# Kernel tuning notes

Measured on AMD Instinct MI355X. Metric: run time of the kernel, lower is better.

The kernel has to match this reference:

```python
import jax, jax.numpy as jnp
import numpy as np

N = 50000      # nodes
E = 800000     # edges (before self-loops)
IN = 128       # in_channels
HID = 64       # hidden_channels
OUT = 64       # out_channels
G = 512        # number of graphs in the batch


def _glorot(key, shape):
    fan_in, fan_out = shape[0], shape[-1]
    s = jnp.sqrt(6.0 / (fan_in + fan_out))
    return jax.random.uniform(key, shape, jnp.float32, -s, s)


def setup_inputs() -> dict:
    key = jax.random.key(0)
    ks = jax.random.split(key, 16)
    x = jax.random.normal(ks[0], (N, IN), jnp.float32)
    edge_index = jax.random.randint(ks[1], (2, E), 0, N, jnp.int64)
    batch = jnp.sort(jax.random.randint(ks[2], (N,), 0, G, jnp.int64))
    return {
        "x": x,
        "edge_index": edge_index,
        "batch": batch,
        # GCNConv(IN, HID)
        "W1": _glorot(ks[3], (IN, HID)),
        "b1": jnp.zeros((HID,), jnp.float32),
        # GATConv(HID, HID, heads=2, concat=True)
        "W2": _glorot(ks[4], (HID, 2 * HID)),
        "a_src2": _glorot(ks[5], (2, HID)),
        "a_dst2": _glorot(ks[6], (2, HID)),
        "b2": jnp.zeros((2 * HID,), jnp.float32),
        # GATConv(2*HID, OUT, heads=1, concat=False)
        "W3": _glorot(ks[7], (2 * HID, OUT)),
        "a_src3": _glorot(ks[8], (1, OUT)),
        "a_dst3": _glorot(ks[9], (1, OUT)),
        "b3": jnp.zeros((OUT,), jnp.float32),
        # fc: Linear(OUT, 2)
        "Wfc": _glorot(ks[10], (OUT, 2)),
        "bfc": jnp.zeros((2,), jnp.float32),
    }


def _add_self_loops(src, dst, n):
    loop = jnp.arange(n, dtype=src.dtype)
    return jnp.concatenate([src, loop]), jnp.concatenate([dst, loop])


def _gcn_conv(x, src, dst, W, b):
    # src -> dst message passing with symmetric normalization (self-loops included)
    n = x.shape[0]
    h = x @ W                                      # [N, F]
    deg = jax.ops.segment_sum(jnp.ones(src.shape[0], h.dtype), dst, num_segments=n)
    dis = jnp.where(deg > 0, jax.lax.rsqrt(jnp.maximum(deg, 1e-12)), 0.0)
    norm = dis[src] * dis[dst]                     # [E']
    out = jax.ops.segment_sum(h[src] * norm[:, None], dst, num_segments=n)
    return out + b


def _gat_conv(x, src, dst, W, a_src, a_dst, b, heads, outc, concat):
    n = x.shape[0]
    h = (x @ W).reshape(n, heads, outc)            # [N, H, F]
    al_s = (h * a_src).sum(-1)                     # [N, H] from source nodes
    al_d = (h * a_dst).sum(-1)                     # [N, H] from target nodes
    e = jax.nn.leaky_relu(al_s[src] + al_d[dst], 0.2)   # [E', H]
    emax = jax.ops.segment_max(e, dst, num_segments=n)  # every node has a self-loop
    ex = jnp.exp(e - emax[dst])
    den = jax.ops.segment_sum(ex, dst, num_segments=n)
    alpha = ex / den[dst]                          # segment softmax over incoming edges
    out = jax.ops.segment_sum(h[src] * alpha[..., None], dst, num_segments=n)
    out = out.reshape(n, heads * outc) if concat else out.mean(axis=1)
    return out + b


def reference(x, edge_index, batch, W1, b1, W2, a_src2, a_dst2, b2,
              W3, a_src3, a_dst3, b3, Wfc, bfc):
    n = x.shape[0]
    src, dst = _add_self_loops(edge_index[0], edge_index[1], n)
    h = jax.nn.relu(_gcn_conv(x, src, dst, W1, b1))            # dropout = identity (eval)
    h = jax.nn.relu(_gat_conv(h, src, dst, W2, a_src2, a_dst2, b2, 2, HID, True))
    h = _gat_conv(h, src, dst, W3, a_src3, a_dst3, b3, 1, OUT, False)
    # global mean pool over graphs
    sums = jax.ops.segment_sum(h, batch, num_segments=G)
    cnts = jax.ops.segment_sum(jnp.ones((n,), h.dtype), batch, num_segments=G)
    pooled = sums / jnp.maximum(cnts, 1.0)[:, None]            # [G, OUT]
    logits = pooled @ Wfc + bfc                                # [G, 2]
    return jax.nn.log_softmax(logits, axis=1)
```

## Files before the change

kernel.cpp:

```cpp
#include <hip/hip_runtime.h>
#include <hip/hip_bf16.h>
#include <hip/hip_fp16.h>
#include <math.h>

#define BDIM 256

using v8h = __attribute__((ext_vector_type(8))) _Float16;
using v4f = __attribute__((ext_vector_type(4))) float;

#define NB  512
#define CH  8192
#define CAP 4096
#define PS  8


__device__ __forceinline__ float wave_max64(float v) {
#pragma unroll
  for (int o = 32; o > 0; o >>= 1) v = fmaxf(v, __shfl_xor(v, o, 64));
  return v;
}
__device__ __forceinline__ float wave_sum64(float v) {
#pragma unroll
  for (int o = 32; o > 0; o >>= 1) v += __shfl_xor(v, o, 64);
  return v;
}

__device__ __forceinline__ float leaky02(float v) {
  return v >= 0.0f ? v : 0.2f * v;
}

template <int KIN, int KOUT, bool A_FP32, int HEADS, bool SCALE>
__launch_bounds__(BDIM) __global__
void gemm_mfma(const void* __restrict__ Ap, const float* __restrict__ W,
               _Float16* __restrict__ C, const float* __restrict__ rs,
               const float* __restrict__ a_src, const float* __restrict__ a_dst,
               float* __restrict__ al_s, float* __restrict__ al_d, int N) {
  constexpr int KP = KIN + 8;
  constexpr int NT = KOUT / 16;
  __shared__ _Float16 Wt[KOUT * KP];
  int tid = threadIdx.x;
  for (int i = tid; i < KIN * KOUT; i += BDIM) {
    int k = i / KOUT, n = i % KOUT;
    Wt[n * KP + k] = (_Float16)W[i];
  }
  __syncthreads();
  int lane = tid & 63;
  int quad = lane >> 4, l16 = lane & 15;
  int m0 = blockIdx.x * 64 + (tid >> 6) * 16;
  if (m0 >= N) return;
  v4f acc[NT];
#pragma unroll
  for (int nt = 0; nt < NT; ++nt) acc[nt] = (v4f){0.0f, 0.0f, 0.0f, 0.0f};
#pragma unroll
  for (int k0 = 0; k0 < KIN; k0 += 32) {
    v8h a;
    if constexpr (A_FP32) {
      const float* ap = (const float*)Ap + (size_t)(m0 + l16) * KIN + k0 + quad * 8;
#pragma unroll
      for (int j = 0; j < 8; ++j) a[j] = (_Float16)ap[j];
    } else {
      a = *(const v8h*)((const _Float16*)Ap + (size_t)(m0 + l16) * KIN + k0 + quad * 8);
    }
#pragma unroll
    for (int nt = 0; nt < NT; ++nt) {
      v8h b = *(const v8h*)&Wt[(nt * 16 + l16) * KP + k0 + quad * 8];
      acc[nt] = __builtin_amdgcn_mfma_f32_16x16x32_f16(a, b, acc[nt], 0, 0, 0);
    }
  }
  float sc[4];
#pragma unroll
  for (int r = 0; r < 4; ++r) sc[r] = SCALE ? rs[m0 + quad * 4 + r] : 1.0f;
#pragma unroll
  for (int nt = 0; nt < NT; ++nt)
#pragma unroll
    for (int r = 0; r < 4; ++r)
      C[(size_t)(m0 + quad * 4 + r) * KOUT + nt * 16 + l16] =
          (_Float16)(acc[nt][r] * sc[r]);

  if constexpr (HEADS > 0) {
    constexpr int TPH = NT / HEADS;
    constexpr int FPH = KOUT / HEADS;
    float av_s[NT], av_d[NT];
#pragma unroll
    for (int nt = 0; nt < NT; ++nt) {
      int head = nt / TPH, c = (nt % TPH) * 16 + l16;
      av_s[nt] = a_src[head * FPH + c];
      av_d[nt] = a_dst[head * FPH + c];
    }
#pragma unroll
    for (int r = 0; r < 4; ++r) {
#pragma unroll
      for (int head = 0; head < HEADS; ++head) {
        float ps = 0.0f, pd = 0.0f;
#pragma unroll
        for (int t = 0; t < TPH; ++t) {
          int nt = head * TPH + t;
          ps += acc[nt][r] * av_s[nt];
          pd += acc[nt][r] * av_d[nt];
        }
#pragma unroll
        for (int o = 1; o < 16; o <<= 1) {
          ps += __shfl_xor(ps, o, 64);
          pd += __shfl_xor(pd, o, 64);
        }
        if (l16 == 0) {
          int row = m0 + quad * 4 + r;
          al_s[(size_t)head * N + row] = ps;
          al_d[(size_t)head * N + row] = pd;
        }
      }
    }
  }
}


__launch_bounds__(BDIM) __global__
void hist_a(const int* __restrict__ ei, int E, int TOT, int bw,
            int* __restrict__ counts, int nWG) {
  __shared__ int hist[NB];
  int tid = threadIdx.x, wg = blockIdx.x;
  for (int i = tid; i < NB; i += BDIM) hist[i] = 0;
  __syncthreads();
  int base = wg * CH, lim = min(CH, TOT - base);
  for (int i = tid; i < lim; i += BDIM) {
    int e = base + i;
    int dst = (e < E) ? ei[E + e] : (e - E);
    atomicAdd(&hist[dst / bw], 1);
  }
  __syncthreads();
  for (int b = tid; b < NB; b += BDIM) counts[(size_t)b * nWG + wg] = hist[b];
}

__launch_bounds__(BDIM) __global__
void scan_bucket(const int* __restrict__ counts, int nWG,
                 int* __restrict__ off, int* __restrict__ btot) {
  int b = blockIdx.x * (BDIM / 64) + (threadIdx.x >> 6);
  int lane = threadIdx.x & 63;
  if (b >= NB) return;
  const int* c = counts + (size_t)b * nWG;
  int* o = off + (size_t)b * nWG;
  int carry = 0;
  for (int base = 0; base < nWG; base += 64) {
    int i = base + lane;
    int v = (i < nWG) ? c[i] : 0;
    int incl = v;
#pragma unroll
    for (int s = 1; s < 64; s <<= 1) {
      int t = __shfl_up(incl, s, 64);
      if (lane >= s) incl += t;
    }
    if (i < nWG) o[i] = carry + incl - v;
    carry += __shfl(incl, 63, 64);
  }
  if (lane == 0) btot[b] = carry;
}

__launch_bounds__(512) __global__
void scan_tot(const int* __restrict__ btot, int* __restrict__ bbase,
              int* __restrict__ row_ptr, int N, int TOT) {
  __shared__ int wsum[8], wpre[8];
  int tid = threadIdx.x, lane = tid & 63, w = tid >> 6;
  int v = btot[tid];
  int incl = v;
#pragma unroll
  for (int o = 1; o < 64; o <<= 1) {
    int t = __shfl_up(incl, o, 64);
    if (lane >= o) incl += t;
  }
  if (lane == 63) wsum[w] = incl;
  __syncthreads();
  if (w == 0 && lane < 8) {
    int s = wsum[lane];
#pragma unroll
    for (int o = 1; o < 8; o <<= 1) {
      int t = __shfl_up(s, o, 64);
      if (lane >= o) s += t;
    }
    wpre[lane] = s - wsum[lane];
  }
  __syncthreads();
  bbase[tid] = wpre[w] + incl - v;
  if (tid == 0) { bbase[NB] = TOT; row_ptr[N] = TOT; }
}

__launch_bounds__(BDIM) __global__
void bucket_b(const int* __restrict__ ei, int E, int TOT, int bw,
              const int* __restrict__ off, const int* __restrict__ bbase,
              int nWG, unsigned int* __restrict__ ebuf) {
  __shared__ int cur[NB];
  int tid = threadIdx.x, wg = blockIdx.x;
  for (int b = tid; b < NB; b += BDIM)
    cur[b] = bbase[b] + off[(size_t)b * nWG + wg];
  __syncthreads();
  int base = wg * CH, lim = min(CH, TOT - base);
  for (int i = tid; i < lim; i += BDIM) {
    int e = base + i;
    int src, dst;
    if (e < E) { src = ei[e]; dst = ei[E + e]; }
    else       { src = dst = e - E; }
    int b = dst / bw;
    int pos = atomicAdd(&cur[b], 1);
    ebuf[pos] = ((unsigned int)(dst - b * bw) << 17) | (unsigned int)src;
  }
}

__launch_bounds__(BDIM) __global__
void csr_c(const unsigned int* __restrict__ ebuf, const int* __restrict__ bbase,
           int N, int bw,
           int* __restrict__ row_ptr, float* __restrict__ dis,
           int* __restrict__ csr_src) {
  __shared__ unsigned int eb[CAP];
  __shared__ unsigned int ob[CAP];
  __shared__ int cnt[128], loff[128], cur[128];
  int tid = threadIdx.x, b = blockIdx.x;
  int d0 = b * bw;
  if (d0 >= N) return;
  int width = min(bw, N - d0);
  int sbase = bbase[b];
  int send = bbase[b + 1];
  int nb = send - sbase;
  if (tid < 128) cnt[tid] = 0;
  __syncthreads();
  for (int i = tid; i < nb; i += BDIM) {
    unsigned int v = ebuf[sbase + i];
    eb[i] = v;
    atomicAdd(&cnt[v >> 17], 1);
  }
  __syncthreads();
  if (tid < 64) {
    int c0 = cnt[tid * 2], c1 = cnt[tid * 2 + 1];
    int s = c0 + c1;
    int incl = s;
#pragma unroll
    for (int o = 1; o < 64; o <<= 1) {
      int t = __shfl_up(incl, o, 64);
      if (tid >= o) incl += t;
    }
    int excl = incl - s;
    loff[tid * 2] = excl;
    loff[tid * 2 + 1] = excl + c0;
  }
  __syncthreads();
  if (tid < width) {
    row_ptr[d0 + tid] = sbase + loff[tid];
    dis[d0 + tid] = rsqrtf((float)cnt[tid]);
    cur[tid] = loff[tid];
  }
  __syncthreads();
  for (int i = tid; i < nb; i += BDIM) {
    unsigned int v = eb[i];
    int p = atomicAdd(&cur[v >> 17], 1);
    ob[p] = v & 0x1FFFFu;
  }
  __syncthreads();
  for (int i = tid; i < nb; i += BDIM) csr_src[sbase + i] = (int)ob[i];
}

__launch_bounds__(BDIM) __global__
void gcn_gather(const __half* __restrict__ h, const int* __restrict__ row_ptr,
                const int* __restrict__ csr_src, const float* __restrict__ dis,
                const float* __restrict__ b, __half* __restrict__ out, int N) {
  constexpr int U = 8;
  int wid = blockIdx.x * (BDIM / 64) + (threadIdx.x >> 6);
  int lane = threadIdx.x & 63;
  if (wid >= N) return;
  int beg = row_ptr[wid], end = row_ptr[wid + 1];
  float acc = 0.0f;
  for (int base = beg; base < end; base += 64) {
    int nch = min(64, end - base);
    int s_l = (lane < nch) ? csr_src[base + lane] : 0;
    int jfull = nch & ~(U - 1);
    for (int j = 0; j < jfull; j += U) {
      int ss[U]; __half vv[U];
#pragma unroll
      for (int u = 0; u < U; ++u) ss[u] = __shfl(s_l, j + u, 64);
#pragma unroll
      for (int u = 0; u < U; ++u) vv[u] = h[(size_t)ss[u] * 64 + lane];
#pragma unroll
      for (int u = 0; u < U; ++u) acc += __half2float(vv[u]);
    }
    for (int j = jfull; j < nch; ++j) {
      int s = __shfl(s_l, j, 64);
      acc += __half2float(h[(size_t)s * 64 + lane]);
    }
  }
  out[(size_t)wid * 64 + lane] = __float2half(fmaxf(acc * dis[wid] + b[lane], 0.0f));
}

__launch_bounds__(BDIM) __global__
void gat_fused2(const __half* __restrict__ h, const int* __restrict__ row_ptr,
                const int* __restrict__ csr_src, const float* __restrict__ al_s,
                const float* __restrict__ al_d, const float* __restrict__ b,
                __half* __restrict__ out, int N) {
  constexpr int U = 8;
  int wid = blockIdx.x * (BDIM / 64) + (threadIdx.x >> 6);
  int lane = threadIdx.x & 63;
  if (wid >= N) return;
  int head = lane >> 5;
  const __half2* hrow = (const __half2*)h;
  int beg = row_ptr[wid], end = row_ptr[wid + 1];
  int deg = end - beg;
  float ad0 = al_d[wid], ad1 = al_d[(size_t)N + wid];
  float accx = 0.0f, accy = 0.0f, l0, l1;
  if (deg <= 64) {
    int s_l = (lane < deg) ? csr_src[beg + lane] : 0;
    float e0 = (lane < deg) ? leaky02(al_s[s_l] + ad0) : -3.4e38f;
    float e1 = (lane < deg) ? leaky02(al_s[(size_t)N + s_l] + ad1) : -3.4e38f;
    float m0 = wave_max64(e0), m1 = wave_max64(e1);
    float ex0 = (lane < deg) ? expf(e0 - m0) : 0.0f;
    float ex1 = (lane < deg) ? expf(e1 - m1) : 0.0f;
    l0 = wave_sum64(ex0);
    l1 = wave_sum64(ex1);
    int jmax = (deg + U - 1) & ~(U - 1);
    for (int j = 0; j < jmax; j += U) {
      int ss[U]; float aa[U]; __half2 vv[U];
#pragma unroll
      for (int u = 0; u < U; ++u) {
        ss[u] = __shfl(s_l, j + u, 64);
        float a0 = __shfl(ex0, j + u, 64);
        float a1 = __shfl(ex1, j + u, 64);
        aa[u] = head ? a1 : a0;
      }
#pragma unroll
      for (int u = 0; u < U; ++u) vv[u] = hrow[(size_t)ss[u] * 64 + lane];
#pragma unroll
      for (int u = 0; u < U; ++u) {
        float2 v = __half22float2(vv[u]);
        accx += aa[u] * v.x;
        accy += aa[u] * v.y;
      }
    }
  } else {
    float m0 = -3.4e38f, m1 = -3.4e38f;
    for (int base = beg; base < end; base += 64) {
      int nch = min(64, end - base);
      int s = (lane < nch) ? csr_src[base + lane] : 0;
      float e0 = (lane < nch) ? leaky02(al_s[s] + ad0) : -3.4e38f;
      float e1 = (lane < nch) ? leaky02(al_s[(size_t)N + s] + ad1) : -3.4e38f;
      m0 = fmaxf(m0, wave_max64(e0));
      m1 = fmaxf(m1, wave_max64(e1));
    }
    l0 = l1 = 0.0f;
    for (int base = beg; base < end; base += 64) {
      int nch = min(64, end - base);
      int s_l = (lane < nch) ? csr_src[base + lane] : 0;
      float ex0 = 0.0f, ex1 = 0.0f;
      if (lane < nch) {
        ex0 = expf(leaky02(al_s[s_l] + ad0) - m0);
        ex1 = expf(leaky02(al_s[(size_t)N + s_l] + ad1) - m1);
      }
      l0 += wave_sum64(ex0);
      l1 += wave_sum64(ex1);
      int jmax = (nch + U - 1) & ~(U - 1);
      for (int j = 0; j < jmax; j += U) {
        int ss[U]; float aa[U]; __half2 vv[U];
#pragma unroll
        for (int u = 0; u < U; ++u) {
          ss[u] = __shfl(s_l, j + u, 64);
          float a0 = __shfl(ex0, j + u, 64);
          float a1 = __shfl(ex1, j + u, 64);
          aa[u] = head ? a1 : a0;
        }
#pragma unroll
        for (int u = 0; u < U; ++u) vv[u] = hrow[(size_t)ss[u] * 64 + lane];
#pragma unroll
        for (int u = 0; u < U; ++u) {
          float2 v = __half22float2(vv[u]);
          accx += aa[u] * v.x;
          accy += aa[u] * v.y;
        }
      }
    }
  }
  float dn = head ? l1 : l0;
  const float2* b2v = (const float2*)b;
  float2 bb = b2v[lane];
  float ox = fmaxf(accx / dn + bb.x, 0.0f);
  float oy = fmaxf(accy / dn + bb.y, 0.0f);
  ((__half2*)out)[(size_t)wid * 64 + lane] = __floats2half2_rn(ox, oy);
}

__launch_bounds__(BDIM) __global__
void gat_fused1(const __half* __restrict__ h, const int* __restrict__ row_ptr,
                const int* __restrict__ csr_src, const float* __restrict__ al_s,
                const float* __restrict__ al_d, const float* __restrict__ b,
                __half* __restrict__ out, int N) {
  constexpr int U = 8;
  int wid = blockIdx.x * (BDIM / 64) + (threadIdx.x >> 6);
  int lane = threadIdx.x & 63;
  if (wid >= N) return;
  int beg = row_ptr[wid], end = row_ptr[wid + 1];
  int deg = end - beg;
  float ad = al_d[wid];
  float acc = 0.0f, l;
  if (deg <= 64) {
    int s_l = (lane < deg) ? csr_src[beg + lane] : 0;
    float e = (lane < deg) ? leaky02(al_s[s_l] + ad) : -3.4e38f;
    float m = wave_max64(e);
    float ex = (lane < deg) ? expf(e - m) : 0.0f;
    l = wave_sum64(ex);
    int jmax = (deg + U - 1) & ~(U - 1);
    for (int j = 0; j < jmax; j += U) {
      int ss[U]; float aa[U]; __half vv[U];
#pragma unroll
      for (int u = 0; u < U; ++u) {
        ss[u] = __shfl(s_l, j + u, 64);
        aa[u] = __shfl(ex, j + u, 64);
      }
#pragma unroll
      for (int u = 0; u < U; ++u) vv[u] = h[(size_t)ss[u] * 64 + lane];
#pragma unroll
      for (int u = 0; u < U; ++u) acc += aa[u] * __half2float(vv[u]);
    }
  } else {
    float m = -3.4e38f;
    for (int base = beg; base < end; base += 64) {
      int nch = min(64, end - base);
      int s = (lane < nch) ? csr_src[base + lane] : 0;
      float e = (lane < nch) ? leaky02(al_s[s] + ad) : -3.4e38f;
      m = fmaxf(m, wave_max64(e));
    }
    l = 0.0f;
    for (int base = beg; base < end; base += 64) {
      int nch = min(64, end - base);
      int s_l = (lane < nch) ? csr_src[base + lane] : 0;
      float ex = (lane < nch) ? expf(leaky02(al_s[s_l] + ad) - m) : 0.0f;
      l += wave_sum64(ex);
      int jmax = (nch + U - 1) & ~(U - 1);
      for (int j = 0; j < jmax; j += U) {
        int ss[U]; float aa[U]; __half vv[U];
#pragma unroll
        for (int u = 0; u < U; ++u) {
          ss[u] = __shfl(s_l, j + u, 64);
          aa[u] = __shfl(ex, j + u, 64);
        }
#pragma unroll
        for (int u = 0; u < U; ++u) vv[u] = h[(size_t)ss[u] * 64 + lane];
#pragma unroll
        for (int u = 0; u < U; ++u) acc += aa[u] * __half2float(vv[u]);
      }
    }
  }
  out[(size_t)wid * 64 + lane] = __float2half(acc / l + b[lane]);
}

__device__ __forceinline__ int lower_bound(const int* __restrict__ a, int n, int v) {
  int lo = 0, hi = n;
  while (lo < hi) {
    int mid = (lo + hi) >> 1;
    if (a[mid] < v) lo = mid + 1; else hi = mid;
  }
  return lo;
}

__launch_bounds__(BDIM) __global__
void pool_partial(const __half* __restrict__ x3, const int* __restrict__ batch,
                  float* __restrict__ part, int N, int G) {
  int wid = blockIdx.x * (BDIM / 64) + (threadIdx.x >> 6);
  int lane = threadIdx.x & 63;
  if (wid >= G * PS) return;
  int g = wid / PS, s = wid % PS;
  int beg = lower_bound(batch, N, g);
  int end = lower_bound(batch, N, g + 1);
  int len = end - beg;
  int lo = beg + (int)((long long)len * s / PS);
  int hi = beg + (int)((long long)len * (s + 1) / PS);
  float acc = 0.0f;
  int n = lo;
  for (; n + 4 <= hi; n += 4) {
    float a0 = __half2float(x3[(size_t)(n + 0) * 64 + lane]);
    float a1 = __half2float(x3[(size_t)(n + 1) * 64 + lane]);
    float a2 = __half2float(x3[(size_t)(n + 2) * 64 + lane]);
    float a3 = __half2float(x3[(size_t)(n + 3) * 64 + lane]);
    acc += (a0 + a1) + (a2 + a3);
  }
  for (; n < hi; ++n) acc += __half2float(x3[(size_t)n * 64 + lane]);
  part[(size_t)wid * 64 + lane] = acc;
}

__launch_bounds__(BDIM) __global__
void pool_head(const float* __restrict__ part, const int* __restrict__ batch,
               const float* __restrict__ Wfc, const float* __restrict__ bfc,
               float* __restrict__ out, int N, int G) {
  int wid = blockIdx.x * (BDIM / 64) + (threadIdx.x >> 6);
  int lane = threadIdx.x & 63;
  if (wid >= G) return;
  float acc = 0.0f;
#pragma unroll
  for (int s = 0; s < PS; ++s) acc += part[((size_t)wid * PS + s) * 64 + lane];
  int beg = lower_bound(batch, N, wid);
  int end = lower_bound(batch, N, wid + 1);
  float p = (end > beg) ? acc / (float)(end - beg) : 0.0f;
  float l0 = wave_sum64(p * Wfc[lane * 2 + 0]);
  float l1 = wave_sum64(p * Wfc[lane * 2 + 1]);
  if (lane == 0) {
    l0 += bfc[0];
    l1 += bfc[1];
    float m = fmaxf(l0, l1);
    float ls = m + logf(expf(l0 - m) + expf(l1 - m));
    out[wid * 2 + 0] = l0 - ls;
    out[wid * 2 + 1] = l1 - ls;
  }
}


static inline int cdiv(int a, int b) { return (a + b - 1) / b; }

extern "C" void kernel_launch(void* const* d_in, const int* in_sizes, int n_in,
                              void* d_out, int out_size, void* d_ws, size_t ws_size,
                              hipStream_t stream) {
  const float* x      = (const float*)d_in[0];
  const int*   ei     = (const int*)d_in[1];
  const int*   batch  = (const int*)d_in[2];
  const float* W1     = (const float*)d_in[3];
  const float* b1     = (const float*)d_in[4];
  const float* W2     = (const float*)d_in[5];
  const float* a_src2 = (const float*)d_in[6];
  const float* a_dst2 = (const float*)d_in[7];
  const float* b2     = (const float*)d_in[8];
  const float* W3     = (const float*)d_in[9];
  const float* a_src3 = (const float*)d_in[10];
  const float* a_dst3 = (const float*)d_in[11];
  const float* b3     = (const float*)d_in[12];
  const float* Wfc    = (const float*)d_in[13];
  const float* bfc    = (const float*)d_in[14];
  float* out = (float*)d_out;

  const int N = in_sizes[2];
  const int E = in_sizes[1] / 2;
  const int G = out_size / 2;
  const int TOT = E + N;
  const int bw  = cdiv(N, NB);
  const int nWG = cdiv(TOT, CH);
  const int M   = NB * nWG;

  char* wsb = (char*)d_ws;
  __half* h1    = (__half*)wsb;
  __half* h2    = h1 + (size_t)N * 64;
  __half* out1h = h2 + (size_t)N * 128;
  __half* out2h = out1h + (size_t)N * 64;
  __half* out3h = out2h + (size_t)N * 128;
  float*  dis   = (float*)(out3h + (size_t)N * 64);
  float*  al_s  = dis + N;
  float*  al_d  = al_s + (size_t)N * 2;
  float*  part  = al_d + (size_t)N * 2;
  int* counts   = (int*)(part + (size_t)G * PS * 64);
  int* off      = counts + M;
  int* btot     = off + M;
  int* bbase    = btot + NB;
  unsigned int* ebuf = (unsigned int*)(bbase + NB + 1);
  int* csr_src  = (int*)(ebuf + TOT);
  int* row_ptr  = csr_src + TOT;

  hist_a<<<nWG, BDIM, 0, stream>>>(ei, E, TOT, bw, counts, nWG);
  scan_bucket<<<cdiv(NB, 4), BDIM, 0, stream>>>(counts, nWG, off, btot);
  scan_tot<<<1, 512, 0, stream>>>(btot, bbase, row_ptr, N, TOT);
  bucket_b<<<nWG, BDIM, 0, stream>>>(ei, E, TOT, bw, off, bbase, nWG, ebuf);
  csr_c<<<NB, BDIM, 0, stream>>>(ebuf, bbase, N, bw, row_ptr, dis, csr_src);

  gemm_mfma<128, 64, true, 0, true><<<cdiv(N, 64), BDIM, 0, stream>>>(
      x, W1, (_Float16*)h1, dis, nullptr, nullptr, nullptr, nullptr, N);
  gcn_gather<<<cdiv(N, 4), BDIM, 0, stream>>>(h1, row_ptr, csr_src, dis, b1, out1h, N);

  gemm_mfma<64, 128, false, 2, false><<<cdiv(N, 64), BDIM, 0, stream>>>(
      out1h, W2, (_Float16*)h2, nullptr, a_src2, a_dst2, al_s, al_d, N);
  gat_fused2<<<cdiv(N, 4), BDIM, 0, stream>>>(h2, row_ptr, csr_src, al_s, al_d,
                                              b2, out2h, N);

  __half* h3 = h2;
  gemm_mfma<128, 64, false, 1, false><<<cdiv(N, 64), BDIM, 0, stream>>>(
      out2h, W3, (_Float16*)h3, nullptr, a_src3, a_dst3, al_s, al_d, N);
  gat_fused1<<<cdiv(N, 4), BDIM, 0, stream>>>(h3, row_ptr, csr_src, al_s, al_d,
                                              b3, out3h, N);

  pool_partial<<<cdiv(G * PS, 4), BDIM, 0, stream>>>(out3h, batch, part, N, G);
  pool_head<<<cdiv(G, 4), BDIM, 0, stream>>>(part, batch, Wfc, bfc, out, N, G);
}
```

Baseline: 288.2 us.

## Gather multiple edges per wave with 16-byte vector loads in GNN aggregation kernels

The three per-node gather kernels (GCN, two-head GAT, one-head GAT) now split each wave into lane groups. Each group handles a different incoming edge and each lane loads 8 fp16 features with one 16-byte load, instead of every lane loading one or two halves per edge serially. Partial sums are combined across groups with xor-shuffle reductions, and a few lanes write vectorized outputs. This cuts the number of load instructions and serial loop iterations per edge. The cost is the extra cross-lane reduction and idle lanes when the masked tail is partly filled.

Result: faster. 277.6 us (-3.7%).

```diff
diff --git a/kernel.cpp b/kernel.cpp
--- a/kernel.cpp
+++ b/kernel.cpp
@@ -260,31 +260,39 @@
 void gcn_gather(const __half* __restrict__ h, const int* __restrict__ row_ptr,
                 const int* __restrict__ csr_src, const float* __restrict__ dis,
                 const float* __restrict__ b, __half* __restrict__ out, int N) {
-  constexpr int U = 8;
   int wid = blockIdx.x * (BDIM / 64) + (threadIdx.x >> 6);
   int lane = threadIdx.x & 63;
   if (wid >= N) return;
+  int grp = lane >> 3;
+  int fb = (lane & 7) * 8;
   int beg = row_ptr[wid], end = row_ptr[wid + 1];
-  float acc = 0.0f;
+  float acc[8];
+#pragma unroll
+  for (int k = 0; k < 8; ++k) acc[k] = 0.0f;
   for (int base = beg; base < end; base += 64) {
     int nch = min(64, end - base);
     int s_l = (lane < nch) ? csr_src[base + lane] : 0;
-    int jfull = nch & ~(U - 1);
-    for (int j = 0; j < jfull; j += U) {
-      int ss[U]; __half vv[U];
-#pragma unroll
-      for (int u = 0; u < U; ++u) ss[u] = __shfl(s_l, j + u, 64);
-#pragma unroll
-      for (int u = 0; u < U; ++u) vv[u] = h[(size_t)ss[u] * 64 + lane];
-#pragma unroll
-      for (int u = 0; u < U; ++u) acc += __half2float(vv[u]);
-    }
-    for (int j = jfull; j < nch; ++j) {
-      int s = __shfl(s_l, j, 64);
-      acc += __half2float(h[(size_t)s * 64 + lane]);
-    }
-  }
-  out[(size_t)wid * 64 + lane] = __float2half(fmaxf(acc * dis[wid] + b[lane], 0.0f));
+    for (int j = 0; j < nch; j += 8) {
+      int idx = j + grp;
+      int s = __shfl(s_l, idx, 64);
+      float w = (idx < nch) ? 1.0f : 0.0f;
+      v8h v = *(const v8h*)((const _Float16*)h + (size_t)s * 64 + fb);
+#pragma unroll
+      for (int k = 0; k < 8; ++k) acc[k] += w * (float)v[k];
+    }
+  }
+#pragma unroll
+  for (int o = 8; o < 64; o <<= 1)
+#pragma unroll
+    for (int k = 0; k < 8; ++k) acc[k] += __shfl_xor(acc[k], o, 64);
+  if (lane < 8) {
+    float dd = dis[wid];
+    v8h ov;
+#pragma unroll
+    for (int k = 0; k < 8; ++k)
+      ov[k] = (_Float16)fmaxf(acc[k] * dd + b[fb + k], 0.0f);
+    *(v8h*)((_Float16*)out + (size_t)wid * 64 + fb) = ov;
+  }
 }
 
 __launch_bounds__(BDIM) __global__
@@ -292,16 +300,19 @@
                 const int* __restrict__ csr_src, const float* __restrict__ al_s,
                 const float* __restrict__ al_d, const float* __restrict__ b,
                 __half* __restrict__ out, int N) {
-  constexpr int U = 8;
   int wid = blockIdx.x * (BDIM / 64) + (threadIdx.x >> 6);
   int lane = threadIdx.x & 63;
   if (wid >= N) return;
-  int head = lane >> 5;
-  const __half2* hrow = (const __half2*)h;
+  int grp = lane >> 4;
+  int fb = (lane & 15) * 8;
+  int hb = (lane & 15) >> 3;
   int beg = row_ptr[wid], end = row_ptr[wid + 1];
   int deg = end - beg;
   float ad0 = al_d[wid], ad1 = al_d[(size_t)N + wid];
-  float accx = 0.0f, accy = 0.0f, l0, l1;
+  float acc[8];
+#pragma unroll
+  for (int k = 0; k < 8; ++k) acc[k] = 0.0f;
+  float l0, l1;
   if (deg <= 64) {
     int s_l = (lane < deg) ? csr_src[beg + lane] : 0;
     float e0 = (lane < deg) ? leaky02(al_s[s_l] + ad0) : -3.4e38f;
@@ -311,24 +322,15 @@
     float ex1 = (lane < deg) ? expf(e1 - m1) : 0.0f;
     l0 = wave_sum64(ex0);
     l1 = wave_sum64(ex1);
-    int jmax = (deg + U - 1) & ~(U - 1);
-    for (int j = 0; j < jmax; j += U) {
-      int ss[U]; float aa[U]; __half2 vv[U];
-#pragma unroll
-      for (int u = 0; u < U; ++u) {
-        ss[u] = __shfl(s_l, j + u, 64);
-        float a0 = __shfl(ex0, j + u, 64);
-        float a1 = __shfl(ex1, j + u, 64);
-        aa[u] = head ? a1 : a0;
-      }
-#pragma unroll
-      for (int u = 0; u < U; ++u) vv[u] = hrow[(size_t)ss[u] * 64 + lane];
-#pragma unroll
-      for (int u = 0; u < U; ++u) {
-        float2 v = __half22float2(vv[u]);
-        accx += aa[u] * v.x;
-        accy += aa[u] * v.y;
-      }
+    for (int j = 0; j < deg; j += 4) {
+      int idx = j + grp;
+      int s = __shfl(s_l, idx, 64);
+      float a0 = __shfl(ex0, idx, 64);
+      float a1 = __shfl(ex1, idx, 64);
+      float a = hb ? a1 : a0;
+      v8h v = *(const v8h*)((const _Float16*)h + (size_t)s * 128 + fb);
+#pragma unroll
+      for (int k = 0; k < 8; ++k) acc[k] += a * (float)v[k];
     }
   } else {
     float m0 = -3.4e38f, m1 = -3.4e38f;
@@ -351,33 +353,30 @@
       }
       l0 += wave_sum64(ex0);
       l1 += wave_sum64(ex1);
-      int jmax = (nch + U - 1) & ~(U - 1);
-      for (int j = 0; j < jmax; j += U) {
-        int ss[U]; float aa[U]; __half2 vv[U];
-#pragma unroll
-        for (int u = 0; u < U; ++u) {
-          ss[u] = __shfl(s_l, j + u, 64);
-          float a0 = __shfl(ex0, j + u, 64);
-          float a1 = __shfl(ex1, j + u, 64);
-          aa[u] = head ? a1 : a0;
-        }
-#pragma unroll
-        for (int u = 0; u < U; ++u) vv[u] = hrow[(size_t)ss[u] * 64 + lane];
-#pragma unroll
-        for (int u = 0; u < U; ++u) {
-          float2 v = __half22float2(vv[u]);
-          accx += aa[u] * v.x;
-          accy += aa[u] * v.y;
-        }
+      for (int j = 0; j < nch; j += 4) {
+        int idx = j + grp;
+        int s = __shfl(s_l, idx, 64);
+        float a0 = __shfl(ex0, idx, 64);
+        float a1 = __shfl(ex1, idx, 64);
+        float a = hb ? a1 : a0;
+        v8h v = *(const v8h*)((const _Float16*)h + (size_t)s * 128 + fb);
+#pragma unroll
+        for (int k = 0; k < 8; ++k) acc[k] += a * (float)v[k];
       }
     }
   }
-  float dn = head ? l1 : l0;
-  const float2* b2v = (const float2*)b;
-  float2 bb = b2v[lane];
-  float ox = fmaxf(accx / dn + bb.x, 0.0f);
-  float oy = fmaxf(accy / dn + bb.y, 0.0f);
-  ((__half2*)out)[(size_t)wid * 64 + lane] = __floats2half2_rn(ox, oy);
+#pragma unroll
+  for (int o = 16; o < 64; o <<= 1)
+#pragma unroll
+    for (int k = 0; k < 8; ++k) acc[k] += __shfl_xor(acc[k], o, 64);
+  if (lane < 16) {
+    float dn = hb ? l1 : l0;
+    v8h ov;
+#pragma unroll
+    for (int k = 0; k < 8; ++k)
+      ov[k] = (_Float16)fmaxf(acc[k] / dn + b[fb + k], 0.0f);
+    *(v8h*)((_Float16*)out + (size_t)wid * 128 + fb) = ov;
+  }
 }
 
 __launch_bounds__(BDIM) __global__
@@ -385,32 +384,31 @@
                 const int* __restrict__ csr_src, const float* __restrict__ al_s,
                 const float* __restrict__ al_d, const float* __restrict__ b,
                 __half* __restrict__ out, int N) {
-  constexpr int U = 8;
   int wid = blockIdx.x * (BDIM / 64) + (threadIdx.x >> 6);
   int lane = threadIdx.x & 63;
   if (wid >= N) return;
+  int grp = lane >> 3;
+  int fb = (lane & 7) * 8;
   int beg = row_ptr[wid], end = row_ptr[wid + 1];
   int deg = end - beg;
   float ad = al_d[wid];
-  float acc = 0.0f, l;
+  float acc[8];
+#pragma unroll
+  for (int k = 0; k < 8; ++k) acc[k] = 0.0f;
+  float l;
   if (deg <= 64) {
     int s_l = (lane < deg) ? csr_src[beg + lane] : 0;
     float e = (lane < deg) ? leaky02(al_s[s_l] + ad) : -3.4e38f;
     float m = wave_max64(e);
     float ex = (lane < deg) ? expf(e - m) : 0.0f;
     l = wave_sum64(ex);
-    int jmax = (deg + U - 1) & ~(U - 1);
-    for (int j = 0; j < jmax; j += U) {
-      int ss[U]; float aa[U]; __half vv[U];
-#pragma unroll
-      for (int u = 0; u < U; ++u) {
-        ss[u] = __shfl(s_l, j + u, 64);
-        aa[u] = __shfl(ex, j + u, 64);
-      }
-#pragma unroll
-      for (int u = 0; u < U; ++u) vv[u] = h[(size_t)ss[u] * 64 + lane];
-#pragma unroll
-      for (int u = 0; u < U; ++u) acc += aa[u] * __half2float(vv[u]);
+    for (int j = 0; j < deg; j += 8) {
+      int idx = j + grp;
+      int s = __shfl(s_l, idx, 64);
+      float a = __shfl(ex, idx, 64);
+      v8h v = *(const v8h*)((const _Float16*)h + (size_t)s * 64 + fb);
+#pragma unroll
+      for (int k = 0; k < 8; ++k) acc[k] += a * (float)v[k];
     }
   } else {
     float m = -3.4e38f;
@@ -426,22 +424,27 @@
       int s_l = (lane < nch) ? csr_src[base + lane] : 0;
       float ex = (lane < nch) ? expf(leaky02(al_s[s_l] + ad) - m) : 0.0f;
       l += wave_sum64(ex);
-      int jmax = (nch + U - 1) & ~(U - 1);
-      for (int j = 0; j < jmax; j += U) {
-        int ss[U]; float aa[U]; __half vv[U];
-#pragma unroll
-        for (int u = 0; u < U; ++u) {
-          ss[u] = __shfl(s_l, j + u, 64);
-          aa[u] = __shfl(ex, j + u, 64);
-        }
-#pragma unroll
-        for (int u = 0; u < U; ++u) vv[u] = h[(size_t)ss[u] * 64 + lane];
-#pragma unroll
-        for (int u = 0; u < U; ++u) acc += aa[u] * __half2float(vv[u]);
+      for (int j = 0; j < nch; j += 8) {
+        int idx = j + grp;
+        int s = __shfl(s_l, idx, 64);
+        float a = __shfl(ex, idx, 64);
+        v8h v = *(const v8h*)((const _Float16*)h + (size_t)s * 64 + fb);
+#pragma unroll
+        for (int k = 0; k < 8; ++k) acc[k] += a * (float)v[k];
       }
     }
   }
-  out[(size_t)wid * 64 + lane] = __float2half(acc / l + b[lane]);
+#pragma unroll
+  for (int o = 8; o < 64; o <<= 1)
+#pragma unroll
+    for (int k = 0; k < 8; ++k) acc[k] += __shfl_xor(acc[k], o, 64);
+  if (lane < 8) {
+    v8h ov;
+#pragma unroll
+    for (int k = 0; k < 8; ++k)
+      ov[k] = (_Float16)(acc[k] / l + b[fb + k]);
+    *(v8h*)((_Float16*)out + (size_t)wid * 64 + fb) = ov;
+  }
 }
 
 __device__ __forceinline__ int lower_bound(const int* __restrict__ a, int n, int v) {
```
